# Performance work log

Measured on AMD Instinct MI355X. Metric: run time of the kernel, lower is better.

Reference implementation:

```python
import jax, jax.numpy as jnp
import numpy as np

N_NODES, N_RELS, N_EDGES, D = 50000, 500, 800000, 128
ALPHA = 0.2  # LeakyReLU negative slope
EPS = 1e-12


def setup_inputs() -> dict:
    key = jax.random.key(0)
    ks = jax.random.split(key, 7)
    ent = jax.random.normal(ks[0], (N_NODES, D), jnp.float32)
    rel = jax.random.normal(ks[1], (N_RELS, D), jnp.float32)
    edge_list = jax.random.randint(ks[2], (2, N_EDGES), 0, N_NODES, dtype=jnp.int64)
    rel_list = jax.random.randint(ks[3], (N_EDGES,), 0, N_RELS, dtype=jnp.int64)
    # learned params (xavier-uniform-scale normal init)
    a = jax.random.normal(ks[4], (D, 3 * D), jnp.float32) * (2.0 / (D + 3 * D)) ** 0.5
    a_2 = jax.random.normal(ks[5], (D,), jnp.float32) * (2.0 / (D + 1)) ** 0.5
    W_r = jax.random.normal(ks[6], (D, D), jnp.float32) * (2.0 / (2 * D)) ** 0.5
    return dict(ent_embedding=ent, rel_embedding=rel, edge_list=edge_list,
                rel_list=rel_list, a=a, a_2=a_2, W_r=W_r)


def reference(ent_embedding, rel_embedding, edge_list, rel_list, a, a_2, W_r):
    ent, rel = ent_embedding, rel_embedding
    N, d = ent.shape
    row, col = edge_list[0], edge_list[1]  # messages aggregated onto `row`
    a_src, a_dst, a_rel = a[:, :d], a[:, d:2 * d], a[:, 2 * d:]
    # edge message: a @ [h_src; h_dst; h_rel]  -> [E, d]  (avoid materializing the concat)
    edge_m = ent[row] @ a_src.T + ent[col] @ a_dst.T + rel[rel_list] @ a_rel.T
    powers = -jax.nn.leaky_relu(edge_m @ a_2, ALPHA)   # [E]
    edge_e = jnp.exp(powers)                           # unnormalized attention (as in KBGAT)
    e_rowsum = jax.ops.segment_sum(edge_e, row, num_segments=N)            # [N]
    h_num = jax.ops.segment_sum(edge_e[:, None] * edge_m, row, num_segments=N)  # [N, d]
    h_prime = h_num / (e_rowsum[:, None] + EPS)
    # concat=True -> ELU; SpGAT then applies dropout (identity in eval) + ReLU
    out_ent = jax.nn.relu(jax.nn.elu(h_prime))
    out_rel = jax.nn.relu(rel @ W_r) + rel
    return out_ent, out_rel
```

## Files before the change

### kernel.cpp

```cpp
#include <hip/hip_runtime.h>
#include <hip/hip_bf16.h>

#define N_NODES 50000
#define N_RELS  500
#define N_EDGES 800000
#define DIM     128
#define BUCKET  64

typedef __attribute__((ext_vector_type(8))) short bf16x8;
typedef __attribute__((ext_vector_type(4))) float f32x4;

static __device__ __forceinline__ short f2bf(float x) {
    __hip_bfloat16 h = __float2bfloat16(x);
    return *reinterpret_cast<short*>(&h);
}

__global__ void build_Bt(const float* __restrict__ a, short* __restrict__ Bt) {
    int t = blockIdx.x * 256 + threadIdx.x;
    int j = t >> 7, k = t & 127;
    const float v = (j < 128) ? a[j * 384 + k] : a[(j - 128) * 384 + 128 + k];
    Bt[t] = f2bf(v);
}

__global__ __launch_bounds__(256) void proj_kernel(const float* __restrict__ ent,
                                                   const short* __restrict__ Bt,
                                                   const float* __restrict__ a2,
                                                   float* __restrict__ projS,
                                                   __hip_bfloat16* __restrict__ projD,
                                                   float* __restrict__ sdot,
                                                   float* __restrict__ ddot) {
    const int wave = threadIdx.x >> 6;
    const int lane = threadIdx.x & 63;
    const int m    = lane & 15;
    const int quad = lane >> 4;
    const int node0 = blockIdx.x * 16;
    const int cbase = wave * 64;

    const float* arow = ent + (size_t)(node0 + m) * DIM + quad * 8;
    bf16x8 afrag[4];
#pragma unroll
    for (int kt = 0; kt < 4; kt++) {
        const float4 lo = *(const float4*)(arow + kt * 32);
        const float4 hi = *(const float4*)(arow + kt * 32 + 4);
        afrag[kt] = (bf16x8){f2bf(lo.x), f2bf(lo.y), f2bf(lo.z), f2bf(lo.w),
                             f2bf(hi.x), f2bf(hi.y), f2bf(hi.z), f2bf(hi.w)};
    }

    f32x4 acc[4];
#pragma unroll
    for (int nt = 0; nt < 4; nt++) acc[nt] = (f32x4){0.f, 0.f, 0.f, 0.f};

#pragma unroll
    for (int kt = 0; kt < 4; kt++) {
#pragma unroll
        for (int nt = 0; nt < 4; nt++) {
            const bf16x8 bfrag = *(const bf16x8*)(Bt + (size_t)(cbase + nt * 16 + m) * DIM
                                                     + kt * 32 + quad * 8);
            acc[nt] = __builtin_amdgcn_mfma_f32_16x16x32_bf16(afrag[kt], bfrag, acc[nt],
                                                              0, 0, 0);
        }
    }

    float part[4] = {0.f, 0.f, 0.f, 0.f};
#pragma unroll
    for (int nt = 0; nt < 4; nt++) {
        const int gc = cbase + nt * 16 + m;
        const float aw = a2[gc & 127];
#pragma unroll
        for (int reg = 0; reg < 4; reg++) {
            const int nd = node0 + quad * 4 + reg;
            const float v = acc[nt][reg];
            if (cbase < 128) projS[(size_t)nd * DIM + gc] = v;
            else             projD[(size_t)nd * DIM + (gc - 128)] = __float2bfloat16(v);
            part[reg] = fmaf(aw, v, part[reg]);
        }
    }
#pragma unroll
    for (int reg = 0; reg < 4; reg++) {
#pragma unroll
        for (int msk = 8; msk >= 1; msk >>= 1) part[reg] += __shfl_xor(part[reg], msk, 64);
    }
    __shared__ float red[4][16];
    if (m == 0) {
#pragma unroll
        for (int reg = 0; reg < 4; reg++) red[wave][quad * 4 + reg] = part[reg];
    }
    __syncthreads();
    const int t = threadIdx.x;
    if (t < 16)       sdot[node0 + t]        = red[0][t] + red[1][t];
    else if (t < 32)  ddot[node0 + (t - 16)] = red[2][t - 16] + red[3][t - 16];
}

__global__ __launch_bounds__(128) void rel_kernel(const float* __restrict__ rel,
                                                  const float* __restrict__ a,
                                                  const float* __restrict__ Wr,
                                                  const float* __restrict__ a2,
                                                  float* __restrict__ rel_proj,
                                                  float* __restrict__ rdot,
                                                  float* __restrict__ out_rel) {
    __shared__ float sR[DIM];
    __shared__ float rp[2];
    const int r = blockIdx.x, i = threadIdx.x;
    sR[i] = rel[r * DIM + i];
    __syncthreads();
    float acc1 = 0.f, acc2 = 0.f;
    const float* arow = a + i * 384 + 256;
#pragma unroll 4
    for (int k = 0; k < DIM; k++) {
        acc1 = fmaf(sR[k], arow[k], acc1);
        acc2 = fmaf(sR[k], Wr[k * DIM + i], acc2);
    }
    rel_proj[r * DIM + i] = acc1;
    out_rel[r * DIM + i] = fmaxf(acc2, 0.f) + sR[i];

    float v = acc1 * a2[i];
#pragma unroll
    for (int m = 32; m >= 1; m >>= 1) v += __shfl_xor(v, m, 64);
    if ((i & 63) == 0) rp[i >> 6] = v;
    __syncthreads();
    if (i == 0) rdot[r] = rp[0] + rp[1];
}

__global__ __launch_bounds__(256) void scatter_kernel(const int* __restrict__ edges,
                                                      const int* __restrict__ rels,
                                                      int* __restrict__ count,
                                                      unsigned* __restrict__ edat) {
    const int e = blockIdx.x * 256 + threadIdx.x;
    if (e < N_EDGES) {
        const int row = edges[e];
        const int col = edges[N_EDGES + e];
        const int rid = rels[e];
        const int pos = atomicAdd(&count[row], 1);
        if (pos < BUCKET)
            edat[(size_t)row * BUCKET + pos] = (unsigned)col | ((unsigned)rid << 16);
    }
}

__global__ __launch_bounds__(256) void gather_kernel(const int* __restrict__ count,
                                                     const unsigned* __restrict__ edat,
                                                     const unsigned short* __restrict__ projD,
                                                     const float* __restrict__ relp,
                                                     const float* __restrict__ sdot,
                                                     const float* __restrict__ ddot,
                                                     const float* __restrict__ rdot,
                                                     float* __restrict__ out) {
    const int wave = threadIdx.x >> 6;
    const int lane = threadIdx.x & 63;
    const int n = blockIdx.x * 4 + wave;
    if (n >= N_NODES) return;

    const int cnt = min(count[n], BUCKET);
    const unsigned ent = edat[(size_t)n * BUCKET + lane];
    const int half = lane >> 5;
    const int d = (lane & 31) * 4;

    float ev_own;
    {
        const float p = sdot[n] + ddot[ent & 0xFFFF] + rdot[ent >> 16];
        ev_own = __expf((p > 0.f) ? -p : -0.2f * p);
    }

    float4 acc = make_float4(0.f, 0.f, 0.f, 0.f);
    float esum = 0.f;
    for (int j = 0; j < cnt; j += 8) {
        unsigned pk[4];
        float    ek[4];
#pragma unroll
        for (int k = 0; k < 4; k++) {
            const int idx = j + 2 * k + half;
            const bool val = idx < cnt;
            pk[k] = val ? (unsigned)__shfl((int)ent, idx, 64) : 0u;
            ek[k] = val ? __shfl(ev_own, idx, 64) : 0.f;
        }
        uint2  uk[4];
        float4 rk[4];
#pragma unroll
        for (int k = 0; k < 4; k++) {
            uk[k] = *(const uint2*)(projD + (((size_t)(pk[k] & 0xFFFF)) << 7) + d);
            rk[k] = *(const float4*)(relp + (((size_t)(pk[k] >> 16)) << 7) + d);
        }
#pragma unroll
        for (int k = 0; k < 4; k++) {
            acc.x = fmaf(ek[k], __uint_as_float(uk[k].x << 16)         + rk[k].x, acc.x);
            acc.y = fmaf(ek[k], __uint_as_float(uk[k].x & 0xFFFF0000u) + rk[k].y, acc.y);
            acc.z = fmaf(ek[k], __uint_as_float(uk[k].y << 16)         + rk[k].z, acc.z);
            acc.w = fmaf(ek[k], __uint_as_float(uk[k].y & 0xFFFF0000u) + rk[k].w, acc.w);
            esum += ek[k];
        }
    }
    esum  += __shfl_xor(esum, 32, 64);
    acc.x += __shfl_xor(acc.x, 32, 64);
    acc.y += __shfl_xor(acc.y, 32, 64);
    acc.z += __shfl_xor(acc.z, 32, 64);
    acc.w += __shfl_xor(acc.w, 32, 64);

    if (half == 0) {
        const float inv = 1.f / (esum + 1e-12f);
        float* op = out + ((size_t)n << 7) + d;
        const float4 sp = *(const float4*)op;
        float4 o;
        o.x = fmaxf(fmaf(sp.x, esum, acc.x) * inv, 0.f);
        o.y = fmaxf(fmaf(sp.y, esum, acc.y) * inv, 0.f);
        o.z = fmaxf(fmaf(sp.z, esum, acc.z) * inv, 0.f);
        o.w = fmaxf(fmaf(sp.w, esum, acc.w) * inv, 0.f);
        *(float4*)op = o;
    }
}

extern "C" void kernel_launch(void* const* d_in, const int* in_sizes, int n_in,
                              void* d_out, int out_size, void* d_ws, size_t ws_size,
                              hipStream_t stream) {
    const float* ent  = (const float*)d_in[0];
    const float* rel  = (const float*)d_in[1];
    const int*   edges = (const int*)d_in[2];
    const int*   rels  = (const int*)d_in[3];
    const float* a    = (const float*)d_in[4];
    const float* a2   = (const float*)d_in[5];
    const float* Wr   = (const float*)d_in[6];

    float* out_ent = (float*)d_out;
    float* out_rel = (float*)d_out + N_NODES * DIM;

    float* relp  = (float*)d_ws;
    float* sdot  = relp + N_RELS * DIM;
    float* ddot  = sdot + N_NODES;
    float* rdot  = ddot + N_NODES;
    short* Bt    = (short*)(rdot + 512);
    unsigned short* projD = (unsigned short*)(Bt + 256 * 128);
    unsigned* edat = (unsigned*)(projD + (size_t)N_NODES * DIM);
    int*   count = (int*)(edat + (size_t)N_NODES * BUCKET);

    hipMemsetAsync(count, 0, N_NODES * sizeof(int), stream);

    build_Bt<<<128, 256, 0, stream>>>(a, Bt);
    proj_kernel<<<N_NODES / 16, 256, 0, stream>>>(ent, Bt, a2, out_ent,
                                                  (__hip_bfloat16*)projD, sdot, ddot);
    rel_kernel<<<N_RELS, 128, 0, stream>>>(rel, a, Wr, a2, relp, rdot, out_rel);

    scatter_kernel<<<(N_EDGES + 255) / 256, 256, 0, stream>>>(edges, rels, count, edat);

    gather_kernel<<<(N_NODES + 3) / 4, 256, 0, stream>>>(count, edat, projD, relp,
                                                         sdot, ddot, rdot, out_ent);
}
```

Measured before the change: 227.8 us.

## Split per-node edge buckets by XCD to localize scatter atomics

The scatter kernel now reads the XCD id from a hardware register and keeps a separate counter and a 16-slot sub-bucket per XCD for each node, so atomics on a given counter come only from one XCD. The gather kernel reads the two 64-entry halves, compacts the valid entries with ballot and popcount into LDS along with their precomputed attention weights, and then runs the same accumulation loop. The aim is to cut cross-die atomic contention and coherence traffic in the scatter step. In exchange, the count array is eight times larger and needs a bigger memset, the edge list is twice as large, and a sub-bucket can overflow at 16 entries, which silently drops edges for high-degree nodes and skewed inputs. The early return for out-of-range nodes was also removed, so the kernel depends on the node count being a multiple of 4.

```diff
diff --git a/kernel.cpp b/kernel.cpp
--- a/kernel.cpp
+++ b/kernel.cpp
@@ -5,7 +5,8 @@
 #define N_RELS  500
 #define N_EDGES 800000
 #define DIM     128
-#define BUCKET  64
+#define SUBCAP  16
+#define SLOTS   128
 
 typedef __attribute__((ext_vector_type(8))) short bf16x8;
 typedef __attribute__((ext_vector_type(4))) float f32x4;
@@ -130,9 +131,11 @@
         const int row = edges[e];
         const int col = edges[N_EDGES + e];
         const int rid = rels[e];
-        const int pos = atomicAdd(&count[row], 1);
-        if (pos < BUCKET)
-            edat[(size_t)row * BUCKET + pos] = (unsigned)col | ((unsigned)rid << 16);
+        const unsigned xcd = __builtin_amdgcn_s_getreg(63508) & 7u;
+        const int pos = atomicAdd(&count[xcd * N_NODES + row], 1);
+        if (pos < SUBCAP)
+            edat[(size_t)row * SLOTS + xcd * SUBCAP + pos] =
+                (unsigned)col | ((unsigned)rid << 16);
     }
 }
 
@@ -144,21 +147,40 @@
                                                      const float* __restrict__ ddot,
                                                      const float* __restrict__ rdot,
                                                      float* __restrict__ out) {
+    __shared__ uint2 lds[4][64];
     const int wave = threadIdx.x >> 6;
     const int lane = threadIdx.x & 63;
     const int n = blockIdx.x * 4 + wave;
-    if (n >= N_NODES) return;
-
-    const int cnt = min(count[n], BUCKET);
-    const unsigned ent = edat[(size_t)n * BUCKET + lane];
+
+    const unsigned ent0 = edat[(size_t)n * SLOTS + lane];
+    const unsigned ent1 = edat[(size_t)n * SLOTS + 64 + lane];
+    const int sub  = lane >> 4;
+    const int slot = lane & 15;
+    const int c0 = min(count[sub * N_NODES + n], SUBCAP);
+    const int c1 = min(count[(4 + sub) * N_NODES + n], SUBCAP);
+    const bool v0 = slot < c0;
+    const bool v1 = slot < c1;
+    const float sdn = sdot[n];
+
+    const float p0 = sdn + ddot[ent0 & 0xFFFF] + rdot[ent0 >> 16];
+    const float p1 = sdn + ddot[ent1 & 0xFFFF] + rdot[ent1 >> 16];
+    const float ev0 = v0 ? __expf((p0 > 0.f) ? -p0 : -0.2f * p0) : 0.f;
+    const float ev1 = v1 ? __expf((p1 > 0.f) ? -p1 : -0.2f * p1) : 0.f;
+
+    const unsigned long long m0 = __ballot(v0);
+    const unsigned long long m1 = __ballot(v1);
+    const unsigned long long below = (1ull << lane) - 1ull;
+    const int base0 = (int)__popcll(m0);
+    const int r0 = (int)__popcll(m0 & below);
+    const int r1 = base0 + (int)__popcll(m1 & below);
+    int cnt = base0 + (int)__popcll(m1);
+    if (v0) lds[wave][r0] = make_uint2(ent0, __float_as_uint(ev0));
+    if (v1 && r1 < 64) lds[wave][r1] = make_uint2(ent1, __float_as_uint(ev1));
+    cnt = min(cnt, 64);
+    __syncthreads();
+
     const int half = lane >> 5;
     const int d = (lane & 31) * 4;
-
-    float ev_own;
-    {
-        const float p = sdot[n] + ddot[ent & 0xFFFF] + rdot[ent >> 16];
-        ev_own = __expf((p > 0.f) ? -p : -0.2f * p);
-    }
 
     float4 acc = make_float4(0.f, 0.f, 0.f, 0.f);
     float esum = 0.f;
@@ -169,8 +191,9 @@
         for (int k = 0; k < 4; k++) {
             const int idx = j + 2 * k + half;
             const bool val = idx < cnt;
-            pk[k] = val ? (unsigned)__shfl((int)ent, idx, 64) : 0u;
-            ek[k] = val ? __shfl(ev_own, idx, 64) : 0.f;
+            const uint2 q = lds[wave][val ? idx : 0];
+            pk[k] = val ? q.x : 0u;
+            ek[k] = val ? __uint_as_float(q.y) : 0.f;
         }
         uint2  uk[4];
         float4 rk[4];
@@ -228,9 +251,9 @@
     short* Bt    = (short*)(rdot + 512);
     unsigned short* projD = (unsigned short*)(Bt + 256 * 128);
     unsigned* edat = (unsigned*)(projD + (size_t)N_NODES * DIM);
-    int*   count = (int*)(edat + (size_t)N_NODES * BUCKET);
-
-    hipMemsetAsync(count, 0, N_NODES * sizeof(int), stream);
+    int*   count = (int*)(edat + (size_t)N_NODES * SLOTS);
+
+    hipMemsetAsync(count, 0, 8 * N_NODES * sizeof(int), stream);
 
     build_Bt<<<128, 256, 0, stream>>>(a, Bt);
     proj_kernel<<<N_NODES / 16, 256, 0, stream>>>(ent, Bt, a2, out_ent,
```

After: 231.3 us. About the same (+1.6%).
